# Optimization experiments

Hardware: AMD Instinct MI355X
Metric: run time of the kernel (lower is better)

The kernel has to match this reference:

```python
import jax, jax.numpy as jnp
import numpy as np

B_SZ, L, D_MODEL = 2, 2048, 1024
EXPAND, N_STATE, K = 2, 16, 4
D_INNER = D_MODEL * EXPAND


def setup_inputs() -> dict:
    key = jax.random.key(0)
    ks = jax.random.split(key, 12)
    s = lambda k, shape, scale=0.02: jax.random.normal(k, shape, jnp.float32) * scale
    return {
        "x": jax.random.normal(ks[0], (B_SZ, L, D_MODEL), jnp.float32),
        "ln_gamma": jnp.ones((D_MODEL,), jnp.float32),
        "ln_beta": jnp.zeros((D_MODEL,), jnp.float32),
        "W_in": s(ks[1], (D_MODEL, 2 * D_INNER)),
        "conv_w": s(ks[2], (D_INNER, 1, K), 0.1),
        "conv_b": jnp.zeros((D_INNER,), jnp.float32),
        "A_log": jax.random.normal(ks[3], (N_STATE,), jnp.float32),
        "B_mat": s(ks[4], (N_STATE, D_INNER), 0.05),
        "C_mat": s(ks[5], (D_INNER, N_STATE), 0.05),
        "D_vec": s(ks[6], (D_INNER,), 0.1),
        "Wd": s(ks[7], (D_INNER, D_INNER)),
        "bd": jnp.zeros((D_INNER,), jnp.float32),
        "W_out": s(ks[8], (D_INNER, D_MODEL)),
    }


def _layernorm(x, g, b, eps=1e-5):
    mu = jnp.mean(x, axis=-1, keepdims=True)
    var = jnp.var(x, axis=-1, keepdims=True)
    return (x - mu) * jax.lax.rsqrt(var + eps) * g + b


def _selective_scan(x, delta, A, B_mat, C_mat, D_vec):
    # x: (b,l,d), delta: (b,l), A: (n,)
    dA = jnp.exp(delta[..., None] * A)            # (b,l,n)
    Bx = jnp.einsum('bld,nd->bln', x, B_mat) * delta[..., None]  # (b,l,n)

    def step(h, inp):
        dA_t, Bx_t = inp
        h = dA_t * h + Bx_t
        return h, h

    h0 = jnp.zeros((x.shape[0], A.shape[0]), x.dtype)
    # scan over seq axis
    _, hs = jax.lax.scan(step, h0, (jnp.swapaxes(dA, 0, 1), jnp.swapaxes(Bx, 0, 1)))
    hs = jnp.swapaxes(hs, 0, 1)                   # (b,l,n)
    return jnp.einsum('bln,dn->bld', hs, C_mat) + D_vec * x


def reference(x, ln_gamma, ln_beta, W_in, conv_w, conv_b, A_log, B_mat, C_mat, D_vec, Wd, bd, W_out):
    residual = x
    h = _layernorm(x, ln_gamma, ln_beta)
    xg = h @ W_in                                  # (b,l,2*d_inner)
    xs, gate = jnp.split(xg, 2, axis=-1)
    # depthwise causal conv (torch pads K-1 both sides then slices [:L] == left pad K-1)
    xc = jnp.swapaxes(xs, 1, 2)                    # (b,d,l)
    xc = jax.lax.conv_general_dilated(
        xc, conv_w, window_strides=(1,), padding=((K - 1, 0),),
        dimension_numbers=('NCH', 'OIH', 'NCH'), feature_group_count=D_INNER)
    xc = xc + conv_b[None, :, None]
    xs = jnp.swapaxes(xc, 1, 2)                    # (b,l,d)
    xs = jax.nn.silu(xs)
    # S4 kernel
    delta = jnp.mean(jax.nn.softplus(xs @ Wd + bd), axis=-1)  # (b,l)
    A = -jnp.exp(A_log)
    y = _selective_scan(xs, delta, A, B_mat, C_mat, D_vec)
    y = y * jax.nn.silu(gate)
    y = y @ W_out
    return residual + y
```

## Files before the change

### kernel.cpp

```cpp
#include <hip/hip_runtime.h>
#include <cstdint>
#include <cstddef>

typedef unsigned short u16;
typedef __attribute__((ext_vector_type(4))) float floatx4;
typedef __attribute__((ext_vector_type(8))) __bf16 bf16x8;

__device__ __forceinline__ float u2f(u16 u) {
    union { unsigned int i; float f; } x;
    x.i = ((unsigned int)u) << 16;
    return x.f;
}
__device__ __forceinline__ u16 f2u(float f) {
    union { float f; unsigned int i; } x;
    x.f = f;
    unsigned int r = x.i + 0x7fffu + ((x.i >> 16) & 1u);
    return (u16)(r >> 16);
}

__device__ __forceinline__ void swz(int bid, int& x, int& y) {
    int xcd = bid & 7;
    int lid = bid >> 3;
    x = lid >> 2;
    y = xcd * 4 + (lid & 3);
}

__device__ __forceinline__ void tr_tile(const float* __restrict__ in, u16* __restrict__ out,
                                        int K, int N, int bx, int by, float* tile ) {
    int n0 = bx * 32, k0 = by * 32;
    int tx = threadIdx.x & 31, ty = threadIdx.x >> 5;
#pragma unroll
    for (int j = 0; j < 4; ++j) {
        int r = ty + j * 8;
        tile[r * 33 + tx] = in[(size_t)(k0 + r) * N + n0 + tx];
    }
    __syncthreads();
#pragma unroll
    for (int j = 0; j < 4; ++j) {
        int r = ty + j * 8;
        out[(size_t)(n0 + r) * K + k0 + tx] = f2u(tile[tx * 33 + r]);
    }
}

__global__ __launch_bounds__(256)
void prep_kernel(const float* __restrict__ W_in, u16* __restrict__ Wt_in,
                 const float* __restrict__ Wd, u16* __restrict__ Wt_ext,
                 const float* __restrict__ W_out, u16* __restrict__ Wt_out,
                 const float* __restrict__ B_mat,
                 const float* __restrict__ x, const float* __restrict__ gamma,
                 const float* __restrict__ beta, u16* __restrict__ h,
                 float* __restrict__ out) {
    __shared__ float tile[32 * 33];
    int blk = blockIdx.x, t = threadIdx.x;
    if (blk < 4096) {
        tr_tile(W_in, Wt_in, 1024, 4096, blk & 127, blk >> 7, tile);
    } else if (blk < 8192) {
        int b2 = blk - 4096;
        tr_tile(Wd, Wt_ext, 2048, 2048, b2 & 63, b2 >> 6, tile);
    } else if (blk < 10240) {
        int b3 = blk - 8192;
        tr_tile(W_out, Wt_out, 2048, 1024, b3 & 31, b3 >> 5, tile);
    } else if (blk < 14336) {
        int r = blk - 10240;
        const float4* xr = (const float4*)(x + (size_t)r * 1024);
        float4 xv = xr[t];
        ((float4*)(out + (size_t)r * 1024))[t] = xv;
        float s = xv.x + xv.y + xv.z + xv.w;
        float ss = xv.x * xv.x + xv.y * xv.y + xv.z * xv.z + xv.w * xv.w;
#pragma unroll
        for (int off = 32; off > 0; off >>= 1) {
            s += __shfl_down(s, off, 64);
            ss += __shfl_down(ss, off, 64);
        }
        __shared__ float rs[4], rss[4], mu_s, ri_s;
        int wave = t >> 6, lane = t & 63;
        if (lane == 0) { rs[wave] = s; rss[wave] = ss; }
        __syncthreads();
        if (t == 0) {
            float S = rs[0] + rs[1] + rs[2] + rs[3];
            float SS = rss[0] + rss[1] + rss[2] + rss[3];
            float mu = S * (1.f / 1024.f);
            float var = SS * (1.f / 1024.f) - mu * mu;
            mu_s = mu;
            ri_s = rsqrtf(fmaxf(var, 0.f) + 1e-5f);
        }
        __syncthreads();
        float mu = mu_s, ri = ri_s;
        float4 gv = ((const float4*)gamma)[t];
        float4 bv = ((const float4*)beta)[t];
        ushort4 o;
        o.x = f2u((xv.x - mu) * ri * gv.x + bv.x);
        o.y = f2u((xv.y - mu) * ri * gv.y + bv.y);
        o.z = f2u((xv.z - mu) * ri * gv.z + bv.z);
        o.w = f2u((xv.w - mu) * ri * gv.w + bv.w);
        ((ushort4*)(h + (size_t)r * 1024))[t] = o;
    } else {
        int idx = (blk - 14336) * 256 + t;
        int row = 2048 + (idx >> 11), col = idx & 2047;
        u16 v = (row < 2064) ? f2u(B_mat[(size_t)(row - 2048) * 2048 + col]) : (u16)0;
        Wt_ext[(size_t)row * 2048 + col] = v;
    }
}

__device__ __forceinline__ void gl_lds16(const u16* g, u16* l) {
    __builtin_amdgcn_global_load_lds(
        (const __attribute__((address_space(1))) void*)g,
        (__attribute__((address_space(3))) void*)l, 16, 0, 0);
}

template <int EPI>
__device__ __forceinline__
void gemm128_body(const u16* __restrict__ A, const u16* __restrict__ Bt,
                  void* __restrict__ out, int M, int N, int K, int Ksub) {
    __shared__ u16 As[128 * 64];
    __shared__ u16 Bs[128 * 64];
    int bx, by;
    swz(blockIdx.x, bx, by);
    const int tid = threadIdx.x;
    const int wave = tid >> 6, lane = tid & 63;
    const int row0 = by * 128, col0 = bx * 128;
    const int koff = blockIdx.y * Ksub;
    const int l16 = lane & 15, q = lane >> 4;
    const int sRow = lane >> 2, sK = (lane & 3) * 8;

    floatx4 acc[4][4];
#pragma unroll
    for (int i = 0; i < 4; ++i)
#pragma unroll
        for (int j = 0; j < 4; ++j) acc[i][j] = (floatx4){0.f, 0.f, 0.f, 0.f};

    const u16* gA = A + (size_t)(row0 + wave * 32 + sRow) * K + koff + sK;
    const u16* gB = Bt + (size_t)(col0 + wave * 32 + sRow) * K + koff + sK;
    u16* lA = As + wave * 1024;
    u16* lB = Bs + wave * 1024;
    const int rowb = (wave >> 1) * 64, colb = (wave & 1) * 64;

    for (int k0 = 0; k0 < Ksub; k0 += 64) {
#pragma unroll
        for (int h = 0; h < 2; ++h) {
            gl_lds16(gA + h * 32, lA + h * 4096);
            gl_lds16(gA + (size_t)16 * K + h * 32, lA + h * 4096 + 512);
            gl_lds16(gB + h * 32, lB + h * 4096);
            gl_lds16(gB + (size_t)16 * K + h * 32, lB + h * 4096 + 512);
        }
        gA += 64; gB += 64;
        __syncthreads();
#pragma unroll
        for (int h = 0; h < 2; ++h) {
            bf16x8 af[4], bfr[4];
#pragma unroll
            for (int mi = 0; mi < 4; ++mi)
                af[mi] = *(const bf16x8*)(As + h * 4096 + (rowb + mi * 16 + l16) * 32 + q * 8);
#pragma unroll
            for (int ni = 0; ni < 4; ++ni)
                bfr[ni] = *(const bf16x8*)(Bs + h * 4096 + (colb + ni * 16 + l16) * 32 + q * 8);
#pragma unroll
            for (int mi = 0; mi < 4; ++mi)
#pragma unroll
                for (int ni = 0; ni < 4; ++ni)
                    acc[mi][ni] = __builtin_amdgcn_mfma_f32_16x16x32_bf16(
                        af[mi], bfr[ni], acc[mi][ni], 0, 0, 0);
        }
        __syncthreads();
    }

    const int mB = row0 + rowb;
    const int nB = col0 + colb + l16;
    if constexpr (EPI == 0) {
        u16* o = (u16*)out;
#pragma unroll
        for (int mi = 0; mi < 4; ++mi)
#pragma unroll
            for (int ni = 0; ni < 4; ++ni)
#pragma unroll
                for (int rr = 0; rr < 4; ++rr)
                    o[(size_t)(mB + mi * 16 + q * 4 + rr) * N + nB + ni * 16] =
                        f2u(acc[mi][ni][rr]);
    } else {
        float* C = (float*)out;
#pragma unroll
        for (int mi = 0; mi < 4; ++mi)
#pragma unroll
            for (int ni = 0; ni < 4; ++ni)
#pragma unroll
                for (int rr = 0; rr < 4; ++rr)
                    atomicAdd(&C[(size_t)(mB + mi * 16 + q * 4 + rr) * N + nB + ni * 16],
                              acc[mi][ni][rr]);
    }
}

__global__ __launch_bounds__(256)
void gemm_xg(const u16* __restrict__ A, const u16* __restrict__ Bt,
             u16* __restrict__ out, int M, int N, int K) {
    gemm128_body<0>(A, Bt, out, M, N, K, K);
}

__global__ __launch_bounds__(256)
void gemm_fin(const u16* __restrict__ A, const u16* __restrict__ Bt,
              void* __restrict__ out, int M, int N, int K, int Ksub) {
    gemm128_body<4>(A, Bt, out, M, N, K, Ksub);
}

__global__ __launch_bounds__(256)
void gemm_delta_sk(const u16* __restrict__ A, const u16* __restrict__ Bt,
                   u16* __restrict__ planes, int M, int N, int K, int Ksub) {
    u16* plane = planes + (size_t)blockIdx.y * M * N;
    gemm128_body<0>(A, Bt, plane, M, N, K, Ksub);
}

__global__ __launch_bounds__(256)
void delta_reduce(const u16* __restrict__ planes, const float* __restrict__ bias,
                  float* __restrict__ dacc, float* __restrict__ Bdotn) {
    const int r = blockIdx.x;
    const int t = threadIdx.x;
    const size_t PL = (size_t)4096 * 2176;
    const u16* p0 = planes + (size_t)r * 2176 + t * 8;
    const u16* p1 = p0 + PL;
    ushort4 a0 = *(const ushort4*)p0;
    ushort4 a1 = *(const ushort4*)(p0 + 4);
    ushort4 b0 = *(const ushort4*)p1;
    ushort4 b1 = *(const ushort4*)(p1 + 4);
    float4 c0 = *(const float4*)(bias + t * 8);
    float4 c1 = *(const float4*)(bias + t * 8 + 4);
    float e[8];
    e[0] = u2f(a0.x) + u2f(b0.x) + c0.x;
    e[1] = u2f(a0.y) + u2f(b0.y) + c0.y;
    e[2] = u2f(a0.z) + u2f(b0.z) + c0.z;
    e[3] = u2f(a0.w) + u2f(b0.w) + c0.w;
    e[4] = u2f(a1.x) + u2f(b1.x) + c1.x;
    e[5] = u2f(a1.y) + u2f(b1.y) + c1.y;
    e[6] = u2f(a1.z) + u2f(b1.z) + c1.z;
    e[7] = u2f(a1.w) + u2f(b1.w) + c1.w;
    float sv = 0.f;
#pragma unroll
    for (int i = 0; i < 8; ++i)
        sv += (e[i] > 20.f) ? e[i] : log1pf(expf(e[i]));
#pragma unroll
    for (int off = 32; off > 0; off >>= 1)
        sv += __shfl_down(sv, off, 64);
    __shared__ float wsum[4];
    const int wave = t >> 6, lane = t & 63;
    if (lane == 0) wsum[wave] = sv;
    __syncthreads();
    if (t == 0) dacc[r] = wsum[0] + wsum[1] + wsum[2] + wsum[3];
    if (t < 16) {
        const u16* q = planes + (size_t)r * 2176 + 2048 + t;
        Bdotn[(size_t)t * 4096 + r] = u2f(*q) + u2f(*(q + PL));
    }
}

__global__ __launch_bounds__(256)
void gemm_delta(const u16* __restrict__ A, const u16* __restrict__ Bt,
                float* __restrict__ dacc, const float* __restrict__ bias,
                float* __restrict__ Bdotn, int M, int N, int K) {
    __shared__ u16 As[128 * 128];
    __shared__ u16 Bs[64 * 128];
    int bx, by;
    swz(blockIdx.x, bx, by);
    const int tid = threadIdx.x;
    const int wave = tid >> 6, lane = tid & 63;
    const int row0 = by * 128, col0 = bx * 64;
    const int l16 = lane & 15, q = lane >> 4;
    const int sRow = lane >> 2, sK = (lane & 3) * 8;

    floatx4 acc[2][4];
#pragma unroll
    for (int i = 0; i < 2; ++i)
#pragma unroll
        for (int j = 0; j < 4; ++j) acc[i][j] = (floatx4){0.f, 0.f, 0.f, 0.f};

    const u16* gA = A + (size_t)(row0 + wave * 32 + sRow) * K + sK;
    const u16* gB = Bt + (size_t)(col0 + wave * 16 + sRow) * K + sK;
    u16* lA = As + wave * 1024;
    u16* lB = Bs + wave * 512;
    const int rowb = wave * 32;

    for (int k0 = 0; k0 < K; k0 += 128) {
#pragma unroll
        for (int h = 0; h < 4; ++h) {
            gl_lds16(gA + h * 32, lA + h * 4096);
            gl_lds16(gA + (size_t)16 * K + h * 32, lA + h * 4096 + 512);
            gl_lds16(gB + h * 32, lB + h * 2048);
        }
        gA += 128; gB += 128;
        __syncthreads();
#pragma unroll
        for (int h = 0; h < 4; ++h) {
            bf16x8 af[2], bfr[4];
#pragma unroll
            for (int mi = 0; mi < 2; ++mi)
                af[mi] = *(const bf16x8*)(As + h * 4096 + (rowb + mi * 16 + l16) * 32 + q * 8);
#pragma unroll
            for (int ni = 0; ni < 4; ++ni)
                bfr[ni] = *(const bf16x8*)(Bs + h * 2048 + (ni * 16 + l16) * 32 + q * 8);
#pragma unroll
            for (int mi = 0; mi < 2; ++mi)
#pragma unroll
                for (int ni = 0; ni < 4; ++ni)
                    acc[mi][ni] = __builtin_amdgcn_mfma_f32_16x16x32_bf16(
                        af[mi], bfr[ni], acc[mi][ni], 0, 0, 0);
        }
        __syncthreads();
    }

    const int mB = row0 + rowb;
    const int nB = col0 + l16;
    if (col0 < 2048) {
#pragma unroll
        for (int mi = 0; mi < 2; ++mi) {
#pragma unroll
            for (int rr = 0; rr < 4; ++rr) {
                float sv = 0.f;
#pragma unroll
                for (int ni = 0; ni < 4; ++ni) {
                    float t2 = acc[mi][ni][rr] + bias[nB + ni * 16];
                    sv += (t2 > 20.f) ? t2 : log1pf(expf(t2));
                }
#pragma unroll
                for (int off = 1; off < 16; off <<= 1)
                    sv += __shfl_xor(sv, off, 64);
                if (l16 == 0)
                    atomicAdd(&dacc[mB + mi * 16 + q * 4 + rr], sv);
            }
        }
    } else {
#pragma unroll
        for (int mi = 0; mi < 2; ++mi)
#pragma unroll
            for (int rr = 0; rr < 4; ++rr)
                Bdotn[(size_t)l16 * 4096 + mB + mi * 16 + q * 4 + rr] =
                    acc[mi][0][rr];
    }
}

__global__ __launch_bounds__(256) void conv_silu_kernel(const u16* __restrict__ xg,
                                                        const float* __restrict__ conv_w,
                                                        const float* __restrict__ conv_b,
                                                        u16* __restrict__ xsc,
                                                        float* __restrict__ delta_acc) {
    int r0 = blockIdx.x * 8;
    int l0 = r0 & 2047, bb = r0 >> 11;
    int t = threadIdx.x, d8 = t * 8;
    if (t < 8) delta_acc[r0 + t] = 0.f;

    ushort4 rw[11][2];
#pragma unroll
    for (int j = 0; j < 11; ++j) {
        int ls = l0 + j - 3;
        if (ls >= 0) {
            const u16* row = xg + (size_t)((bb << 11) + ls) * 4096 + d8;
            rw[j][0] = *(const ushort4*)row;
            rw[j][1] = *(const ushort4*)(row + 4);
        } else {
            rw[j][0] = (ushort4){0, 0, 0, 0};
            rw[j][1] = (ushort4){0, 0, 0, 0};
        }
    }
    float w[8][4];
#pragma unroll
    for (int j = 0; j < 8; ++j) {
        float4 wv = *(const float4*)(conv_w + (size_t)(d8 + j) * 4);
        w[j][0] = wv.x; w[j][1] = wv.y; w[j][2] = wv.z; w[j][3] = wv.w;
    }
    float cb[8];
    {
        float4 b0 = *(const float4*)(conv_b + d8);
        float4 b1 = *(const float4*)(conv_b + d8 + 4);
        cb[0] = b0.x; cb[1] = b0.y; cb[2] = b0.z; cb[3] = b0.w;
        cb[4] = b1.x; cb[5] = b1.y; cb[6] = b1.z; cb[7] = b1.w;
    }
#pragma unroll
    for (int i = 0; i < 8; ++i) {
        float xs[8];
#pragma unroll
        for (int j = 0; j < 8; ++j) xs[j] = cb[j];
#pragma unroll
        for (int k = 0; k < 4; ++k) {
            ushort4 u0 = rw[i + k][0], u1 = rw[i + k][1];
            xs[0] += w[0][k] * u2f(u0.x); xs[1] += w[1][k] * u2f(u0.y);
            xs[2] += w[2][k] * u2f(u0.z); xs[3] += w[3][k] * u2f(u0.w);
            xs[4] += w[4][k] * u2f(u1.x); xs[5] += w[5][k] * u2f(u1.y);
            xs[6] += w[6][k] * u2f(u1.z); xs[7] += w[7][k] * u2f(u1.w);
        }
        ushort4 o0, o1;
        o0.x = f2u(xs[0] / (1.f + expf(-xs[0])));
        o0.y = f2u(xs[1] / (1.f + expf(-xs[1])));
        o0.z = f2u(xs[2] / (1.f + expf(-xs[2])));
        o0.w = f2u(xs[3] / (1.f + expf(-xs[3])));
        o1.x = f2u(xs[4] / (1.f + expf(-xs[4])));
        o1.y = f2u(xs[5] / (1.f + expf(-xs[5])));
        o1.z = f2u(xs[6] / (1.f + expf(-xs[6])));
        o1.w = f2u(xs[7] / (1.f + expf(-xs[7])));
        u16* orow = xsc + (size_t)(r0 + i) * 2048 + d8;
        *(ushort4*)orow = o0;
        *(ushort4*)(orow + 4) = o1;
    }
}

__global__ __launch_bounds__(256) void scan_kernel(const float* __restrict__ delta_acc,
                                                   const float* __restrict__ Bdotn,
                                                   const float* __restrict__ A_log,
                                                   float* __restrict__ hsn) {
    int chain = blockIdx.x;
    int b = chain >> 4, n = chain & 15;
    int t = threadIdx.x;
    int wave = t >> 6, lane = t & 63;
    __shared__ float sd[2048], sb[2048];
    __shared__ float wA[4], wB[4];
#pragma unroll
    for (int m = 0; m < 2; ++m) {
        int idx = (m * 256 + t) * 4;
        *(float4*)(sd + idx) = *(const float4*)(delta_acc + b * 2048 + idx);
        *(float4*)(sb + idx) = *(const float4*)(Bdotn + (size_t)n * 4096 + b * 2048 + idx);
    }
    __syncthreads();
    float An = -expf(A_log[n]);
    int base = t * 8;
    float a[8], bb[8];
#pragma unroll
    for (int i = 0; i < 8; ++i) {
        float dl = sd[base + i] * (1.f / 2048.f);
        a[i] = expf(dl * An);
        bb[i] = sb[base + i] * dl;
    }
    float Aacc = 1.f, Bacc = 0.f;
#pragma unroll
    for (int i = 0; i < 8; ++i) {
        Bacc = a[i] * Bacc + bb[i];
        Aacc = a[i] * Aacc;
    }
#pragma unroll
    for (int d = 1; d < 64; d <<= 1) {
        float Ap = __shfl_up(Aacc, d, 64);
        float Bp = __shfl_up(Bacc, d, 64);
        if (lane >= d) {
            Bacc = Aacc * Bp + Bacc;
            Aacc = Aacc * Ap;
        }
    }
    if (lane == 63) { wA[wave] = Aacc; wB[wave] = Bacc; }
    float eA = __shfl_up(Aacc, 1, 64);
    float eB = __shfl_up(Bacc, 1, 64);
    if (lane == 0) { eA = 1.f; eB = 0.f; }
    __syncthreads();
    float pB = 0.f;
#pragma unroll
    for (int w = 0; w < 3; ++w)
        if (w < wave) pB = wA[w] * pB + wB[w];
    float h = eA * pB + eB;
#pragma unroll
    for (int i = 0; i < 8; ++i) {
        h = a[i] * h + bb[i];
        sd[base + i] = h;
    }
    __syncthreads();
#pragma unroll
    for (int m = 0; m < 2; ++m) {
        int idx = (m * 256 + t) * 4;
        *(float4*)(hsn + (size_t)n * 4096 + b * 2048 + idx) = *(const float4*)(sd + idx);
    }
}

__global__ __launch_bounds__(256) void ymid_kernel(const float* __restrict__ hsn,
                                                   const float* __restrict__ C_mat,
                                                   const float* __restrict__ D_vec,
                                                   const u16* __restrict__ xsc,
                                                   const u16* __restrict__ xg,
                                                   u16* __restrict__ ymid) {
    const int t = threadIdx.x;
    const int d0 = blockIdx.x * 512 + t * 2;
    const int r0 = blockIdx.y * 32;
    __shared__ float hsv[32 * 16];
#pragma unroll
    for (int k = 0; k < 2; ++k) {
        int idx = t * 2 + k;
        int rl = idx >> 4, nn = idx & 15;
        hsv[idx] = hsn[(size_t)nn * 4096 + r0 + rl];
    }
    float c0[16], c1[16];
#pragma unroll
    for (int k = 0; k < 4; ++k) {
        float4 v0 = *(const float4*)(C_mat + (size_t)d0 * 16 + k * 4);
        float4 v1 = *(const float4*)(C_mat + (size_t)(d0 + 1) * 16 + k * 4);
        c0[k * 4 + 0] = v0.x; c0[k * 4 + 1] = v0.y; c0[k * 4 + 2] = v0.z; c0[k * 4 + 3] = v0.w;
        c1[k * 4 + 0] = v1.x; c1[k * 4 + 1] = v1.y; c1[k * 4 + 2] = v1.z; c1[k * 4 + 3] = v1.w;
    }
    const float dv0 = D_vec[d0], dv1 = D_vec[d0 + 1];
    __syncthreads();
#pragma unroll 4
    for (int rl = 0; rl < 32; ++rl) {
        const int r = r0 + rl;
        float h0 = 0.f, h1 = 0.f;
#pragma unroll
        for (int nn = 0; nn < 16; ++nn) {
            float hv = hsv[rl * 16 + nn];
            h0 += hv * c0[nn];
            h1 += hv * c1[nn];
        }
        unsigned int xv = *(const unsigned int*)(xsc + (size_t)r * 2048 + d0);
        unsigned int gv = *(const unsigned int*)(xg + (size_t)r * 4096 + 2048 + d0);
        float x0 = u2f((u16)(xv & 0xffffu)), x1 = u2f((u16)(xv >> 16));
        float g0 = u2f((u16)(gv & 0xffffu)), g1 = u2f((u16)(gv >> 16));
        float y0 = (h0 + dv0 * x0) * (g0 / (1.f + expf(-g0)));
        float y1 = (h1 + dv1 * x1) * (g1 / (1.f + expf(-g1)));
        unsigned int o = (unsigned int)f2u(y0) | ((unsigned int)f2u(y1) << 16);
        *(unsigned int*)(ymid + (size_t)r * 2048 + d0) = o;
    }
}

extern "C" void kernel_launch(void* const* d_in, const int* in_sizes, int n_in,
                              void* d_out, int out_size, void* d_ws, size_t ws_size,
                              hipStream_t stream) {
    (void)in_sizes; (void)n_in;
    const float* x      = (const float*)d_in[0];
    const float* ln_g   = (const float*)d_in[1];
    const float* ln_b   = (const float*)d_in[2];
    const float* W_in   = (const float*)d_in[3];
    const float* conv_w = (const float*)d_in[4];
    const float* conv_b = (const float*)d_in[5];
    const float* A_log  = (const float*)d_in[6];
    const float* B_mat  = (const float*)d_in[7];
    const float* C_mat  = (const float*)d_in[8];
    const float* D_vec  = (const float*)d_in[9];
    const float* Wd     = (const float*)d_in[10];
    const float* bd     = (const float*)d_in[11];
    const float* W_out  = (const float*)d_in[12];
    float* out = (float*)d_out;

    char* base = (char*)d_ws;
    u16* Wt_in  = (u16*)base;
    u16* h_ln   = (u16*)base + 4096ull * 1024;
    u16* ymid   = (u16*)base;
    u16* Wt_ext = (u16*)(base + (16ull << 20));
    u16* Wt_out = (u16*)(base + (25ull << 20));
    u16* xg     = (u16*)(base + (29ull << 20));
    u16* xsc    = (u16*)(base + (61ull << 20));
    float* delta_acc = (float*)(base + (77ull << 20));
    float* Bdotn = delta_acc + 4096;
    float* hsn   = Bdotn + 16 * 4096;
    u16* planes  = (u16*)(base + (78ull << 20));
    size_t needed = (77ull << 20) + 4096ull * 4 * (1 + 2 * 16);
    size_t needed_sk = (78ull << 20) + 2ull * 4096 * 2176 * 2;

    if (needed > ws_size) {
        hipMemsetAsync(d_out, 0x7F, (size_t)out_size * 4, stream);
        return;
    }
    const bool use_sk = (ws_size >= needed_sk);

    prep_kernel<<<14848, 256, 0, stream>>>(W_in, Wt_in, Wd, Wt_ext, W_out, Wt_out,
                                           B_mat, x, ln_g, ln_b, h_ln, out);
    gemm_xg<<<1024, 256, 0, stream>>>(h_ln, Wt_in, xg, 4096, 4096, 1024);
    conv_silu_kernel<<<512, 256, 0, stream>>>(xg, conv_w, conv_b, xsc, delta_acc);
    if (use_sk) {
        gemm_delta_sk<<<dim3(544, 2), 256, 0, stream>>>(xsc, Wt_ext, planes,
                                                        4096, 2176, 2048, 1024);
        delta_reduce<<<4096, 256, 0, stream>>>(planes, bd, delta_acc, Bdotn);
    } else {
        gemm_delta<<<1056, 256, 0, stream>>>(xsc, Wt_ext, delta_acc, bd, Bdotn,
                                             4096, 2112, 2048);
    }
    scan_kernel<<<32, 256, 0, stream>>>(delta_acc, Bdotn, A_log, hsn);
    ymid_kernel<<<dim3(4, 128), 256, 0, stream>>>(hsn, C_mat, D_vec, xsc, xg, ymid);
    gemm_fin<<<dim3(256, 2), 256, 0, stream>>>(ymid, Wt_out, out, 4096, 1024, 2048, 1024);
}
```

Baseline: 333.0 us.

## Replace atomic split-K output GEMM with plane writes plus reduce; vectorize weight transpose

The final output GEMM now writes each split-K half to its own fp32 plane with plain stores, and a separate reduce kernel adds both planes into the output, which already holds the residual. This replaces per-element float atomicAdd traffic. The weight-transpose helper also switches to float4 loads and ushort4 stores. The cost is an extra kernel launch and about 32 MB of extra plane write and read traffic.

```diff
diff --git a/kernel.cpp b/kernel.cpp
--- a/kernel.cpp
+++ b/kernel.cpp
@@ -28,18 +28,21 @@
 __device__ __forceinline__ void tr_tile(const float* __restrict__ in, u16* __restrict__ out,
                                         int K, int N, int bx, int by, float* tile ) {
     int n0 = bx * 32, k0 = by * 32;
-    int tx = threadIdx.x & 31, ty = threadIdx.x >> 5;
-#pragma unroll
-    for (int j = 0; j < 4; ++j) {
-        int r = ty + j * 8;
-        tile[r * 33 + tx] = in[(size_t)(k0 + r) * N + n0 + tx];
-    }
+    int t = threadIdx.x;
+    int r = t >> 3, c4 = (t & 7) * 4;
+    float4 v = *(const float4*)(in + (size_t)(k0 + r) * N + n0 + c4);
+    tile[r * 33 + c4 + 0] = v.x;
+    tile[r * 33 + c4 + 1] = v.y;
+    tile[r * 33 + c4 + 2] = v.z;
+    tile[r * 33 + c4 + 3] = v.w;
     __syncthreads();
-#pragma unroll
-    for (int j = 0; j < 4; ++j) {
-        int r = ty + j * 8;
-        out[(size_t)(n0 + r) * K + k0 + tx] = f2u(tile[tx * 33 + r]);
-    }
+    int n = t >> 3, kg = (t & 7) * 4;
+    ushort4 o;
+    o.x = f2u(tile[(kg + 0) * 33 + n]);
+    o.y = f2u(tile[(kg + 1) * 33 + n]);
+    o.z = f2u(tile[(kg + 2) * 33 + n]);
+    o.w = f2u(tile[(kg + 3) * 33 + n]);
+    *(ushort4*)(out + (size_t)(n0 + n) * K + k0 + kg) = o;
 }
 
 __global__ __launch_bounds__(256)
@@ -176,6 +179,16 @@
                 for (int rr = 0; rr < 4; ++rr)
                     o[(size_t)(mB + mi * 16 + q * 4 + rr) * N + nB + ni * 16] =
                         f2u(acc[mi][ni][rr]);
+    } else if constexpr (EPI == 2) {
+        float* o = (float*)out;
+#pragma unroll
+        for (int mi = 0; mi < 4; ++mi)
+#pragma unroll
+            for (int ni = 0; ni < 4; ++ni)
+#pragma unroll
+                for (int rr = 0; rr < 4; ++rr)
+                    o[(size_t)(mB + mi * 16 + q * 4 + rr) * N + nB + ni * 16] =
+                        acc[mi][ni][rr];
     } else {
         float* C = (float*)out;
 #pragma unroll
@@ -199,6 +212,26 @@
 void gemm_fin(const u16* __restrict__ A, const u16* __restrict__ Bt,
               void* __restrict__ out, int M, int N, int K, int Ksub) {
     gemm128_body<4>(A, Bt, out, M, N, K, Ksub);
+}
+
+__global__ __launch_bounds__(256)
+void gemm_fin_pl(const u16* __restrict__ A, const u16* __restrict__ Bt,
+                 float* __restrict__ planes, int M, int N, int K, int Ksub) {
+    float* plane = planes + (size_t)blockIdx.y * M * N;
+    gemm128_body<2>(A, Bt, plane, M, N, K, Ksub);
+}
+
+__global__ __launch_bounds__(256)
+void fin_reduce(const float* __restrict__ planes, float* __restrict__ out) {
+    const size_t idx = ((size_t)blockIdx.x * 256 + threadIdx.x) * 4;
+    const float4 p0 = *(const float4*)(planes + idx);
+    const float4 p1 = *(const float4*)(planes + (size_t)4096 * 1024 + idx);
+    float4 o = *(const float4*)(out + idx);
+    o.x += p0.x + p1.x;
+    o.y += p0.y + p1.y;
+    o.z += p0.z + p1.z;
+    o.w += p0.w + p1.w;
+    *(float4*)(out + idx) = o;
 }
 
 __global__ __launch_bounds__(256)
@@ -539,6 +572,7 @@
     float* Bdotn = delta_acc + 4096;
     float* hsn   = Bdotn + 16 * 4096;
     u16* planes  = (u16*)(base + (78ull << 20));
+    float* fplanes = (float*)(base + (78ull << 20));
     size_t needed = (77ull << 20) + 4096ull * 4 * (1 + 2 * 16);
     size_t needed_sk = (78ull << 20) + 2ull * 4096 * 2176 * 2;
 
@@ -562,5 +596,11 @@
     }
     scan_kernel<<<32, 256, 0, stream>>>(delta_acc, Bdotn, A_log, hsn);
     ymid_kernel<<<dim3(4, 128), 256, 0, stream>>>(hsn, C_mat, D_vec, xsc, xg, ymid);
-    gemm_fin<<<dim3(256, 2), 256, 0, stream>>>(ymid, Wt_out, out, 4096, 1024, 2048, 1024);
-}
+    if (use_sk) {
+        gemm_fin_pl<<<dim3(256, 2), 256, 0, stream>>>(ymid, Wt_out, fplanes,
+                                                      4096, 1024, 2048, 1024);
+        fin_reduce<<<4096, 256, 0, stream>>>(fplanes, out);
+    } else {
+        gemm_fin<<<dim3(256, 2), 256, 0, stream>>>(ymid, Wt_out, out, 4096, 1024, 2048, 1024);
+    }
+}
```

Result: faster. 324.4 us (-2.6%).
